# Performance work log

Measured on AMD Instinct MI355X. Metric: run time of the kernel, lower is better.

The kernel has to match this reference:

```python
import jax, jax.numpy as jnp
import numpy as np

NUM_HEADS = 32
HEAD_DIM = 128
Q_LORA_RANK = 1536
BSZ = 8
SEQ_LEN = 4096


def setup_inputs() -> dict:
    key = jax.random.key(0)
    k1, k2, k3, k4 = jax.random.split(key, 4)
    hidden_states_q = jax.random.normal(k1, (BSZ, Q_LORA_RANK), dtype=jnp.float32)
    key_value = jax.random.normal(k2, (BSZ, SEQ_LEN, NUM_HEADS, 2 * HEAD_DIM), dtype=jnp.float32)
    # q_proj: Linear(q_lora_rank -> num_heads*head_dim); store weight transposed [in, out]
    W_q = jax.random.normal(k3, (Q_LORA_RANK, NUM_HEADS * HEAD_DIM), dtype=jnp.float32) * (1.0 / np.sqrt(Q_LORA_RANK))
    b_q = jax.random.normal(k4, (NUM_HEADS * HEAD_DIM,), dtype=jnp.float32) * 0.01
    return {"hidden_states_q": hidden_states_q, "key_value": key_value, "W_q": W_q, "b_q": b_q}


def reference(hidden_states_q, key_value, W_q, b_q):
    bsz = hidden_states_q.shape[0]
    # split combined KV cache: [b, s, h, 2d] -> k, v each [b, s, h, d]
    key = key_value[..., :HEAD_DIM]
    value = key_value[..., HEAD_DIM:]
    # q projection: [b, r] @ [r, h*d] -> [b, h, d]
    q = (hidden_states_q @ W_q + b_q).reshape(bsz, NUM_HEADS, HEAD_DIM)
    # attn scores (NO 1/sqrt(d) scaling, matching the original module): [b, h, s]
    attn_scores = jnp.einsum('bhd,bshd->bhs', q, key)
    attn_probs = jax.nn.softmax(attn_scores, axis=-1)
    # weighted value sum: [b, h, d]
    attn_output = jnp.einsum('bhs,bshd->bhd', attn_probs, value)
    return attn_output.reshape(bsz, NUM_HEADS * HEAD_DIM)
```

## Files before the change

### kernel.cpp

```cpp
#include <hip/hip_runtime.h>
#include <math.h>

#define NUM_HEADS 32
#define HEAD_DIM 128
#define QRANK 1536
#define BSZ 8
#define SEQ 4096

__global__ __launch_bounds__(256) void qproj_kernel(
    const float* __restrict__ hq,
    const float* __restrict__ Wq,
    const float* __restrict__ bq,
    float* __restrict__ qout)
{
    __shared__ float lh[BSZ * QRANK];
    __shared__ float red[BSZ][4][64];
    const int t = threadIdx.x;
    for (int i = t; i < BSZ * QRANK; i += 256) lh[i] = hq[i];
    __syncthreads();

    const int nl = t & 63;
    const int ks = t >> 6;
    const int n  = blockIdx.x * 64 + nl;

    float acc[BSZ];
#pragma unroll
    for (int b = 0; b < BSZ; ++b) acc[b] = 0.f;

    const int k0 = ks * (QRANK / 4);
    const int k1 = k0 + (QRANK / 4);
    for (int k = k0; k < k1; ++k) {
        float wv = Wq[(size_t)k * 4096 + n];
#pragma unroll
        for (int b = 0; b < BSZ; ++b) acc[b] += lh[b * QRANK + k] * wv;
    }
#pragma unroll
    for (int b = 0; b < BSZ; ++b) red[b][ks][nl] = acc[b];
    __syncthreads();

    if (ks == 0) {
#pragma unroll
        for (int b = 0; b < BSZ; ++b) {
            float s = red[b][0][nl] + red[b][1][nl] + red[b][2][nl] + red[b][3][nl]
                    + bq[n];
            qout[b * 4096 + n] = s;
        }
    }
}

__global__ __launch_bounds__(1024) void attn_kernel(
    const float* __restrict__ kv,
    const float* __restrict__ q,
    float* __restrict__ out)
{
    __shared__ float  sc[SEQ];
    __shared__ float4 ored[16][2][32];
    __shared__ float  wmaxr[16];
    __shared__ float  wsumr[16];

    const int b    = blockIdx.x >> 5;
    const int h    = blockIdx.x & 31;
    const int tid  = threadIdx.x;
    const int w    = tid >> 6;
    const int lane = tid & 63;
    const int sub  = lane & 31;
    const int half = lane >> 5;

    const float4 qf = *(const float4*)(q + (size_t)b * 4096 + h * 128 + 4 * sub);

    const float4* kv4 = (const float4*)kv;
    const long hb = (long)h * 64;

    for (int it = 0; it < 128; ++it) {
        const int  row = w * 256 + it * 2 + half;
        const long idx = (long)(b * SEQ + row) * 2048 + hb + sub;
        const float4 kf = kv4[idx];
        float p = qf.x * kf.x + qf.y * kf.y + qf.z * kf.z + qf.w * kf.w;
        p += __shfl_xor(p, 1);
        p += __shfl_xor(p, 2);
        p += __shfl_xor(p, 4);
        p += __shfl_xor(p, 8);
        p += __shfl_xor(p, 16);
        if (sub == 0) sc[row] = p;
    }
    __syncthreads();

    float lm = -INFINITY;
    for (int i = tid; i < SEQ; i += 1024) lm = fmaxf(lm, sc[i]);
    lm = fmaxf(lm, __shfl_xor(lm, 1));
    lm = fmaxf(lm, __shfl_xor(lm, 2));
    lm = fmaxf(lm, __shfl_xor(lm, 4));
    lm = fmaxf(lm, __shfl_xor(lm, 8));
    lm = fmaxf(lm, __shfl_xor(lm, 16));
    lm = fmaxf(lm, __shfl_xor(lm, 32));
    if (lane == 0) wmaxr[w] = lm;
    __syncthreads();
    float m = wmaxr[0];
#pragma unroll
    for (int i = 1; i < 16; ++i) m = fmaxf(m, wmaxr[i]);

    float ls = 0.f;
    for (int i = tid; i < SEQ; i += 1024) {
        float p = __expf(sc[i] - m);
        sc[i] = p;
        ls += p;
    }
    ls += __shfl_xor(ls, 1);
    ls += __shfl_xor(ls, 2);
    ls += __shfl_xor(ls, 4);
    ls += __shfl_xor(ls, 8);
    ls += __shfl_xor(ls, 16);
    ls += __shfl_xor(ls, 32);
    if (lane == 0) wsumr[w] = ls;
    __syncthreads();
    float l = 0.f;
#pragma unroll
    for (int i = 0; i < 16; ++i) l += wsumr[i];
    const float invl = 1.f / l;

    float4 acc = make_float4(0.f, 0.f, 0.f, 0.f);
    for (int it = 0; it < 128; ++it) {
        const int  row = w * 256 + it * 2 + half;
        const long idx = (long)(b * SEQ + row) * 2048 + hb + 32 + sub;
        const float4 vf = kv4[idx];
        const float p = sc[row];
        acc.x += p * vf.x;
        acc.y += p * vf.y;
        acc.z += p * vf.z;
        acc.w += p * vf.w;
    }
    ored[w][half][sub] = acc;
    __syncthreads();

    if (tid < 128) {
        const float* of = (const float*)ored;
        float s = 0.f;
#pragma unroll
        for (int i = 0; i < 32; ++i) s += of[i * 128 + tid];
        out[(size_t)b * 4096 + h * 128 + tid] = s * invl;
    }
}

extern "C" void kernel_launch(void* const* d_in, const int* in_sizes, int n_in,
                              void* d_out, int out_size, void* d_ws, size_t ws_size,
                              hipStream_t stream) {
    const float* hq = (const float*)d_in[0];
    const float* kv = (const float*)d_in[1];
    const float* Wq = (const float*)d_in[2];
    const float* bq = (const float*)d_in[3];
    float* outp = (float*)d_out;
    float* qbuf = (float*)d_ws;

    qproj_kernel<<<64, 256, 0, stream>>>(hq, Wq, bq, qbuf);
    attn_kernel<<<BSZ * NUM_HEADS, 1024, 0, stream>>>(kv, qbuf, outp);
}
```

Measured before the change: 1.346 ms.

## Fuse q-projection into attention and use single-pass online softmax over KV

Folds the q projection into the attention kernel: each block computes its own head's 128-wide q slice from W_q, which removes a kernel launch and the workspace round-trip. The attention pass now reads each KV row once, as a full 256-float K|V row, and keeps a per-warp online softmax (running max, sum and rescaled V accumulator) instead of separate score, softmax and value passes. Per-warp partial results are merged with max-rescaling at the end. The cost is redundant W_q reads, since each batch recomputes the projection for its head (8x more W_q traffic), plus two exps per row in every lane.

```diff
diff --git a/kernel.cpp b/kernel.cpp
--- a/kernel.cpp
+++ b/kernel.cpp
@@ -7,56 +7,18 @@
 #define BSZ 8
 #define SEQ 4096
 
-__global__ __launch_bounds__(256) void qproj_kernel(
+__global__ __launch_bounds__(1024) void fused_attn_kernel(
     const float* __restrict__ hq,
+    const float* __restrict__ kv,
     const float* __restrict__ Wq,
     const float* __restrict__ bq,
-    float* __restrict__ qout)
-{
-    __shared__ float lh[BSZ * QRANK];
-    __shared__ float red[BSZ][4][64];
-    const int t = threadIdx.x;
-    for (int i = t; i < BSZ * QRANK; i += 256) lh[i] = hq[i];
-    __syncthreads();
-
-    const int nl = t & 63;
-    const int ks = t >> 6;
-    const int n  = blockIdx.x * 64 + nl;
-
-    float acc[BSZ];
-#pragma unroll
-    for (int b = 0; b < BSZ; ++b) acc[b] = 0.f;
-
-    const int k0 = ks * (QRANK / 4);
-    const int k1 = k0 + (QRANK / 4);
-    for (int k = k0; k < k1; ++k) {
-        float wv = Wq[(size_t)k * 4096 + n];
-#pragma unroll
-        for (int b = 0; b < BSZ; ++b) acc[b] += lh[b * QRANK + k] * wv;
-    }
-#pragma unroll
-    for (int b = 0; b < BSZ; ++b) red[b][ks][nl] = acc[b];
-    __syncthreads();
-
-    if (ks == 0) {
-#pragma unroll
-        for (int b = 0; b < BSZ; ++b) {
-            float s = red[b][0][nl] + red[b][1][nl] + red[b][2][nl] + red[b][3][nl]
-                    + bq[n];
-            qout[b * 4096 + n] = s;
-        }
-    }
-}
-
-__global__ __launch_bounds__(1024) void attn_kernel(
-    const float* __restrict__ kv,
-    const float* __restrict__ q,
     float* __restrict__ out)
 {
-    __shared__ float  sc[SEQ];
-    __shared__ float4 ored[16][2][32];
-    __shared__ float  wmaxr[16];
-    __shared__ float  wsumr[16];
+    __shared__ float  hs[QRANK];
+    __shared__ float  qred[8][128];
+    __shared__ float  qs[HEAD_DIM];
+    __shared__ float4 ow[16][32];
+    __shared__ float  wm[16], wl[16];
 
     const int b    = blockIdx.x >> 5;
     const int h    = blockIdx.x & 31;
@@ -64,80 +26,82 @@
     const int w    = tid >> 6;
     const int lane = tid & 63;
     const int sub  = lane & 31;
-    const int half = lane >> 5;
 
-    const float4 qf = *(const float4*)(q + (size_t)b * 4096 + h * 128 + 4 * sub);
+    for (int i = tid; i < QRANK; i += 1024) hs[i] = hq[b * QRANK + i];
+    __syncthreads();
+
+    {
+        const int c  = tid & 127;
+        const int ks = tid >> 7;
+        const float* wp = Wq + (size_t)(ks * 192) * 4096 + h * 128 + c;
+        float a = 0.f;
+        #pragma unroll 4
+        for (int k = 0; k < 192; ++k) {
+            a += hs[ks * 192 + k] * wp[(size_t)k * 4096];
+        }
+        qred[ks][c] = a;
+    }
+    __syncthreads();
+    if (tid < 128) {
+        float s = bq[h * 128 + tid];
+        #pragma unroll
+        for (int i = 0; i < 8; ++i) s += qred[i][tid];
+        qs[tid] = s;
+    }
+    __syncthreads();
+
+    const float4 qf = *(const float4*)(qs + 4 * sub);
 
     const float4* kv4 = (const float4*)kv;
-    const long hb = (long)h * 64;
+    const size_t base = ((size_t)b * SEQ + (size_t)w * 256) * 2048
+                      + (size_t)h * 64 + lane;
 
-    for (int it = 0; it < 128; ++it) {
-        const int  row = w * 256 + it * 2 + half;
-        const long idx = (long)(b * SEQ + row) * 2048 + hb + sub;
-        const float4 kf = kv4[idx];
-        float p = qf.x * kf.x + qf.y * kf.y + qf.z * kf.z + qf.w * kf.w;
+    float  m = -INFINITY;
+    float  l = 0.f;
+    float4 acc = make_float4(0.f, 0.f, 0.f, 0.f);
+
+    #pragma unroll 4
+    for (int r = 0; r < 256; ++r) {
+        const float4 f = kv4[base + (size_t)r * 2048];
+        float p = qf.x * f.x + qf.y * f.y + qf.z * f.z + qf.w * f.w;
         p += __shfl_xor(p, 1);
         p += __shfl_xor(p, 2);
         p += __shfl_xor(p, 4);
         p += __shfl_xor(p, 8);
         p += __shfl_xor(p, 16);
-        if (sub == 0) sc[row] = p;
+        const float s = __shfl(p, 0);
+
+        const float mn = fmaxf(m, s);
+        const float cs = __expf(m - mn);
+        const float pe = __expf(s - mn);
+        l = l * cs + pe;
+        acc.x = acc.x * cs + pe * f.x;
+        acc.y = acc.y * cs + pe * f.y;
+        acc.z = acc.z * cs + pe * f.z;
+        acc.w = acc.w * cs + pe * f.w;
+        m = mn;
+    }
+
+    if (lane >= 32) {
+        if (lane == 32) { wm[w] = m; wl[w] = l; }
+        ow[w][sub] = acc;
     }
     __syncthreads();
 
-    float lm = -INFINITY;
-    for (int i = tid; i < SEQ; i += 1024) lm = fmaxf(lm, sc[i]);
-    lm = fmaxf(lm, __shfl_xor(lm, 1));
-    lm = fmaxf(lm, __shfl_xor(lm, 2));
-    lm = fmaxf(lm, __shfl_xor(lm, 4));
-    lm = fmaxf(lm, __shfl_xor(lm, 8));
-    lm = fmaxf(lm, __shfl_xor(lm, 16));
-    lm = fmaxf(lm, __shfl_xor(lm, 32));
-    if (lane == 0) wmaxr[w] = lm;
-    __syncthreads();
-    float m = wmaxr[0];
-#pragma unroll
-    for (int i = 1; i < 16; ++i) m = fmaxf(m, wmaxr[i]);
-
-    float ls = 0.f;
-    for (int i = tid; i < SEQ; i += 1024) {
-        float p = __expf(sc[i] - m);
-        sc[i] = p;
-        ls += p;
-    }
-    ls += __shfl_xor(ls, 1);
-    ls += __shfl_xor(ls, 2);
-    ls += __shfl_xor(ls, 4);
-    ls += __shfl_xor(ls, 8);
-    ls += __shfl_xor(ls, 16);
-    ls += __shfl_xor(ls, 32);
-    if (lane == 0) wsumr[w] = ls;
-    __syncthreads();
-    float l = 0.f;
-#pragma unroll
-    for (int i = 0; i < 16; ++i) l += wsumr[i];
-    const float invl = 1.f / l;
-
-    float4 acc = make_float4(0.f, 0.f, 0.f, 0.f);
-    for (int it = 0; it < 128; ++it) {
-        const int  row = w * 256 + it * 2 + half;
-        const long idx = (long)(b * SEQ + row) * 2048 + hb + 32 + sub;
-        const float4 vf = kv4[idx];
-        const float p = sc[row];
-        acc.x += p * vf.x;
-        acc.y += p * vf.y;
-        acc.z += p * vf.z;
-        acc.w += p * vf.w;
-    }
-    ored[w][half][sub] = acc;
-    __syncthreads();
-
     if (tid < 128) {
-        const float* of = (const float*)ored;
-        float s = 0.f;
-#pragma unroll
-        for (int i = 0; i < 32; ++i) s += of[i * 128 + tid];
-        out[(size_t)b * 4096 + h * 128 + tid] = s * invl;
+        float M = wm[0];
+        #pragma unroll
+        for (int i = 1; i < 16; ++i) M = fmaxf(M, wm[i]);
+        float lt = 0.f;
+        float s  = 0.f;
+        #pragma unroll
+        for (int i = 0; i < 16; ++i) {
+            const float sc = __expf(wm[i] - M);
+            lt += wl[i] * sc;
+            const float* of = (const float*)(&ow[i][0]);
+            s += of[tid] * sc;
+        }
+        out[(size_t)b * 4096 + h * 128 + tid] = s / lt;
     }
 }
 
@@ -149,8 +113,7 @@
     const float* Wq = (const float*)d_in[2];
     const float* bq = (const float*)d_in[3];
     float* outp = (float*)d_out;
-    float* qbuf = (float*)d_ws;
+    (void)d_ws; (void)ws_size;
 
-    qproj_kernel<<<64, 256, 0, stream>>>(hq, Wq, bq, qbuf);
-    attn_kernel<<<BSZ * NUM_HEADS, 1024, 0, stream>>>(kv, qbuf, outp);
+    fused_attn_kernel<<<BSZ * NUM_HEADS, 1024, 0, stream>>>(hq, kv, Wq, bq, outp);
 }
```

New measurement: 1.340 ms. About the same (-0.5%).
